# Kernel optimization log

Hardware: AMD Instinct MI355X
Metric: run time of the kernel (lower is better)

The kernel has to match this reference:

```python
import jax, jax.numpy as jnp
import numpy as np

B, S, D = 4, 2048, 384
H, KVH, HD = 6, 2, 64
GROUPS = H // KVH  # 3
ROPE_THETA = 100000.0


def _rope_tables(seq_len, head_dim, theta):
    inv = 1.0 / (theta ** (np.arange(0, head_dim, 2, dtype=np.float32) / head_dim))
    t = np.arange(seq_len, dtype=np.float32)
    freqs = np.outer(t, inv)  # [S, HD//2]
    return jnp.asarray(np.cos(freqs)), jnp.asarray(np.sin(freqs))


def setup_inputs() -> dict:
    key = jax.random.key(0)
    ks = jax.random.split(key, 5)
    hidden_states = jax.random.normal(ks[0], (B, S, D), dtype=jnp.float32)
    Wq = jax.random.normal(ks[1], (D, H * HD), dtype=jnp.float32) * 0.02
    Wk = jax.random.normal(ks[2], (D, KVH * HD), dtype=jnp.float32) * 0.02
    Wv = jax.random.normal(ks[3], (D, KVH * HD), dtype=jnp.float32) * 0.02
    Wo = jax.random.normal(ks[4], (H * HD, D), dtype=jnp.float32) * 0.02
    freqs_cos, freqs_sin = _rope_tables(S, HD, ROPE_THETA)
    return {"hidden_states": hidden_states, "Wq": Wq, "Wk": Wk, "Wv": Wv,
            "Wo": Wo, "freqs_cos": freqs_cos, "freqs_sin": freqs_sin}


def _apply_rope(x, cos, sin):
    # x: [B, S, h, HD]; treat pairs (even, odd) as complex, multiply by e^{i theta}
    xr = x.reshape(*x.shape[:-1], HD // 2, 2)
    x0, x1 = xr[..., 0], xr[..., 1]
    c = cos[None, :, None, :]  # [1, S, 1, HD//2]
    s = sin[None, :, None, :]
    o0 = x0 * c - x1 * s
    o1 = x0 * s + x1 * c
    return jnp.stack([o0, o1], axis=-1).reshape(x.shape)


def reference(hidden_states, Wq, Wk, Wv, Wo, freqs_cos, freqs_sin):
    Bc, Sc, _ = hidden_states.shape
    q = (hidden_states @ Wq).reshape(Bc, Sc, H, HD)
    k = (hidden_states @ Wk).reshape(Bc, Sc, KVH, HD)
    v = (hidden_states @ Wv).reshape(Bc, Sc, KVH, HD)
    q = _apply_rope(q, freqs_cos, freqs_sin)
    k = _apply_rope(k, freqs_cos, freqs_sin)
    # repeat_interleave over the head dim (GQA group broadcast)
    k = jnp.repeat(k, GROUPS, axis=2)  # [B, S, H, HD]
    v = jnp.repeat(v, GROUPS, axis=2)
    scale = 1.0 / jnp.sqrt(jnp.float32(HD))
    scores = jnp.einsum('bqhd,bkhd->bhqk', q, k) * scale  # [B, H, S, S]
    attn = jax.nn.softmax(scores, axis=-1)
    out = jnp.einsum('bhqk,bkhd->bqhd', attn, v)  # [B, S, H, HD]
    out = out.reshape(Bc, Sc, H * HD)
    return out @ Wo
```

## Files before the change

### kernel.cpp

```cpp
#include <hip/hip_runtime.h>
#include <stdint.h>

#define BATCH   4
#define SEQ     2048
#define DMODEL  384
#define NHEAD   6
#define NKVH    2
#define HD      64
#define MTOK    (BATCH*SEQ)
#define NQKV    640
#define QSCALE  (0.125f * 1.4426950408889634f)

typedef __bf16 bf16x8 __attribute__((ext_vector_type(8)));
typedef float  f32x16 __attribute__((ext_vector_type(16)));

__device__ inline unsigned short f2bf(float f) {
  union { float f; unsigned int u; } v; v.f = f;
  return (unsigned short)((v.u + 0x7fffu + ((v.u >> 16) & 1u)) >> 16);
}
__device__ inline float bf2f(unsigned short b) {
  union { unsigned int u; float f; } v; v.u = ((unsigned int)b) << 16;
  return v.f;
}
__device__ inline unsigned int cvtpk(float lo, float hi) {
  unsigned int r;
  asm("v_cvt_pk_bf16_f32 %0, %1, %2" : "=v"(r) : "v"(lo), "v"(hi));
  return r;
}
__device__ inline float exp2_fast(float x) {
  float r;
  asm("v_exp_f32 %0, %1" : "=v"(r) : "v"(x));
  return r;
}

#define GLOAD16(gsrc, ldst) __builtin_amdgcn_global_load_lds( \
    (const __attribute__((address_space(1))) void*)(gsrc), \
    (__attribute__((address_space(3))) void*)(ldst), 16, 0, 0)

__global__ void prep_kernel(const float* __restrict__ X,
                            const float* __restrict__ Wq, const float* __restrict__ Wk,
                            const float* __restrict__ Wv, const float* __restrict__ Wo,
                            unsigned short* __restrict__ Xb,
                            unsigned short* __restrict__ WT,
                            unsigned short* __restrict__ WoT) {
  int idx = blockIdx.x * 256 + threadIdx.x;
  if (idx < (MTOK*DMODEL)/4) {
    float4 v = ((const float4*)X)[idx];
    union { unsigned short s[4]; uint2 u; } o;
    o.s[0] = f2bf(v.x); o.s[1] = f2bf(v.y); o.s[2] = f2bf(v.z); o.s[3] = f2bf(v.w);
    ((uint2*)Xb)[idx] = o.u;
  } else if (idx < (MTOK*DMODEL)/4 + NQKV*DMODEL) {
    int j = idx - (MTOK*DMODEL)/4;
    int n = j / DMODEL, k = j % DMODEL;
    float val = (n < 384) ? Wq[k*384 + n]
              : (n < 512) ? Wk[k*128 + (n-384)]
                          : Wv[k*128 + (n-512)];
    WT[j] = f2bf(val);
  } else if (idx < (MTOK*DMODEL)/4 + NQKV*DMODEL + DMODEL*DMODEL) {
    int j = idx - (MTOK*DMODEL)/4 - NQKV*DMODEL;
    int n = j / DMODEL, k = j % DMODEL;
    WoT[j] = f2bf(Wo[k*384 + n]);
  }
}

template<int NCOLS, bool OUT_BF16, bool ROPE>
__global__ __launch_bounds__(256, 2)
void gemm_kernel(const unsigned short* __restrict__ A,
                 const unsigned short* __restrict__ BT,
                 void* __restrict__ Cout,
                 const float* __restrict__ fcos,
                 const float* __restrict__ fsin) {
  __shared__ unsigned short ldsA[128*64];
  __shared__ unsigned short ldsB[64*64];
  const int tid = threadIdx.x;
  const int wid = tid >> 6, lane = tid & 63;
  const int g = lane >> 5, l31 = lane & 31;
  const int wm = wid >> 1, wn = wid & 1;
  const int mbase = blockIdx.x * 128, nbase = blockIdx.y * 64;

  f32x16 c[2];
  #pragma unroll
  for (int i = 0; i < 2; ++i)
    #pragma unroll
    for (int r = 0; r < 16; ++r) c[i][r] = 0.f;

  for (int kt = 0; kt < DMODEL; kt += 64) {
    #pragma unroll
    for (int i = 0; i < 4; ++i) {
      int L = ((wid*4 + i) << 10) + lane*16;
      int row = L >> 7;
      int slot = (lane & 7) ^ (row & 7);
      GLOAD16(A + (mbase + row)*DMODEL + kt + slot*8, ((char*)ldsA) + L);
    }
    #pragma unroll
    for (int i = 0; i < 2; ++i) {
      int L = ((wid*2 + i) << 10) + lane*16;
      int row = L >> 7;
      int slot = (lane & 7) ^ (row & 7);
      GLOAD16(BT + (nbase + row)*DMODEL + kt + slot*8, ((char*)ldsB) + L);
    }
    __syncthreads();

    bf16x8 bf[4];
    {
      int row = wn*32 + l31;
      #pragma unroll
      for (int s = 0; s < 4; ++s) {
        int slot = ((s<<1) | g) ^ (row & 7);
        bf[s] = *(const bf16x8*)(((const char*)ldsB) + row*128 + slot*16);
      }
    }
    #pragma unroll
    for (int mt = 0; mt < 2; ++mt) {
      int row = wm*64 + mt*32 + l31;
      #pragma unroll
      for (int s = 0; s < 4; ++s) {
        int slot = ((s<<1) | g) ^ (row & 7);
        bf16x8 af = *(const bf16x8*)(((const char*)ldsA) + row*128 + slot*16);
        c[mt] = __builtin_amdgcn_mfma_f32_32x32x16_bf16(af, bf[s], c[mt], 0, 0, 0);
      }
    }
    __syncthreads();
  }

  const int n = nbase + wn*32 + l31;
  const bool isqk = ROPE && (nbase < 512);
  const float rscale = (nbase < 384) ? QSCALE : 1.0f;
  const int ri = (n & 63) >> 1;
  const bool odd = (n & 1) != 0;

  #pragma unroll
  for (int mt = 0; mt < 2; ++mt)
    #pragma unroll
    for (int rr = 0; rr < 16; ++rr) {
      int m = mbase + wm*64 + mt*32 + (rr&3) + ((rr>>2)<<3) + (g<<2);
      float val = c[mt][rr];
      if (isqk) {
        float xp = __shfl_xor(val, 1);
        int s = m & (SEQ-1);
        float cs = fcos[s*32 + ri], sn = fsin[s*32 + ri];
        val = odd ? (xp*sn + val*cs) : (val*cs - xp*sn);
        val *= rscale;
      }
      if (OUT_BF16) ((unsigned short*)Cout)[m*NCOLS + n] = f2bf(val);
      else          ((float*)Cout)[m*NCOLS + n] = val;
    }
}

__global__ void vfrag_kernel(const unsigned short* __restrict__ qkv,
                             unsigned short* __restrict__ Vf) {
  __shared__ unsigned short tile[64][72];
  int t = threadIdx.x;
  int s0 = blockIdx.x * 64;
  int kvh = blockIdx.y;
  int b = blockIdx.z;
  #pragma unroll
  for (int p = 0; p < 2; ++p) {
    int row = (t >> 3) + p*32;
    int c8 = t & 7;
    uint4 v = *(const uint4*)(qkv + (size_t)(b*SEQ + s0 + row)*NQKV + 512 + kvh*64 + c8*8);
    *(uint4*)(&tile[row][c8*8]) = v;
  }
  __syncthreads();
  unsigned short* base = Vf + (size_t)(b*2 + kvh)*131072;
  #pragma unroll
  for (int p = 0; p < 2; ++p) {
    int c = t + p*256;
    int tloc = c >> 8;
    int r = c & 255;
    int dt = r >> 7, sl = (r >> 6) & 1, lane = r & 63;
    int gg = lane >> 5, ll = lane & 31;
    union { unsigned short s[8]; uint4 v; } o;
    #pragma unroll
    for (int j = 0; j < 8; ++j)
      o.s[j] = tile[tloc*32 + sl*16 + gg*8 + j][dt*32 + ll];
    *(uint4*)(base + (size_t)(s0/32 + tloc)*2048 + (dt*2 + sl)*512 + lane*8) = o.v;
  }
}

__device__ __forceinline__ void stage_k(const unsigned short* Kbase, int kv0,
                                        char* kbuf, int lane) {
  #pragma unroll
  for (int i = 0; i < 4; ++i) {
    int L = (i << 10) + lane*16;
    int row = L >> 7;
    int slot = (lane & 7) ^ (row & 7);
    GLOAD16(Kbase + (size_t)(kv0 + row)*NQKV + slot*8, kbuf + L);
  }
}

#define ATTN_BODY(T, VC0, VC1, VC2, VC3, VN0, VN1, VN2, VN3, PREF) do {            \
  if (PREF) {                                                                      \
    stage_k(Kbase, kvbase + ((T)+1)*32, kbuf + (((T)+1)&1)*4096, lane);            \
    const unsigned short* vp = Vfb + (size_t)(part*32 + (T)+1)*2048;               \
    VN0 = *(const bf16x8*)(vp + lane*8);                                           \
    VN1 = *(const bf16x8*)(vp + 512 + lane*8);                                     \
    VN2 = *(const bf16x8*)(vp + 1024 + lane*8);                                    \
    VN3 = *(const bf16x8*)(vp + 1536 + lane*8);                                    \
    asm volatile("s_waitcnt vmcnt(8)" ::: "memory");                               \
  } else {                                                                         \
    asm volatile("s_waitcnt vmcnt(0)" ::: "memory");                               \
  }                                                                                \
  const char* kb = kbuf + ((T)&1)*4096;                                            \
  f32x16 c1;                                                                       \
  _Pragma("unroll")                                                                \
  for (int r = 0; r < 16; ++r) c1[r] = 0.f;                                        \
  _Pragma("unroll")                                                                \
  for (int s = 0; s < 4; ++s) {                                                    \
    int slot = ((s<<1) | g) ^ (l31 & 7);                                           \
    bf16x8 kf = *(const bf16x8*)(kb + l31*128 + slot*16);                          \
    c1 = __builtin_amdgcn_mfma_f32_32x32x16_bf16(kf, qf[s], c1, 0, 0, 0);          \
  }                                                                                \
  float x0 = fmaxf(c1[0],c1[1]), x1 = fmaxf(c1[2],c1[3]);                          \
  float x2 = fmaxf(c1[4],c1[5]), x3 = fmaxf(c1[6],c1[7]);                          \
  float x4 = fmaxf(c1[8],c1[9]), x5 = fmaxf(c1[10],c1[11]);                        \
  float x6 = fmaxf(c1[12],c1[13]), x7 = fmaxf(c1[14],c1[15]);                      \
  float y0 = fmaxf(x0,x1), y1 = fmaxf(x2,x3), y2 = fmaxf(x4,x5), y3 = fmaxf(x6,x7);\
  float pmax = fmaxf(fmaxf(y0,y1), fmaxf(y2,y3));                                  \
  pmax = fmaxf(pmax, __shfl_xor(pmax, 32));                                        \
  if (!__all(pmax <= mrun + 10.f)) {                                               \
    float mnew = fmaxf(mrun, pmax);                                                \
    float alpha = exp2_fast(mrun - mnew);                                          \
    _Pragma("unroll")                                                              \
    for (int r = 0; r < 16; ++r) { acc0[r] *= alpha; acc1[r] *= alpha; }           \
    lrun *= alpha;                                                                 \
    mrun = mnew;                                                                   \
  }                                                                                \
  float p[16];                                                                     \
  _Pragma("unroll")                                                                \
  for (int r = 0; r < 16; ++r) p[r] = exp2_fast(c1[r] - mrun);                     \
  {                                                                                \
    float s0_ = (p[0]+p[1])+(p[2]+p[3]), s1_ = (p[4]+p[5])+(p[6]+p[7]);            \
    float s2_ = (p[8]+p[9])+(p[10]+p[11]), s3_ = (p[12]+p[13])+(p[14]+p[15]);      \
    lrun += (s0_+s1_)+(s2_+s3_);                                                   \
  }                                                                                \
  _Pragma("unroll")                                                                \
  for (int sl = 0; sl < 2; ++sl) {                                                 \
    int rb = sl*8;                                                                 \
    unsigned int w0  = cvtpk(p[rb+0], p[rb+1]);                                    \
    unsigned int w1  = cvtpk(p[rb+2], p[rb+3]);                                    \
    unsigned int wh0 = cvtpk(p[rb+4], p[rb+5]);                                    \
    unsigned int wh1 = cvtpk(p[rb+6], p[rb+7]);                                    \
    unsigned int t0 = g ? w0 : wh0;                                                \
    unsigned int t1 = g ? w1 : wh1;                                                \
    unsigned int r0 = __shfl_xor(t0, 32);                                          \
    unsigned int r1 = __shfl_xor(t1, 32);                                          \
    union { bf16x8 v; unsigned int u[4]; } pf;                                     \
    pf.u[0] = g ? r0  : w0;                                                        \
    pf.u[1] = g ? r1  : w1;                                                        \
    pf.u[2] = g ? wh0 : r0;                                                        \
    pf.u[3] = g ? wh1 : r1;                                                        \
    if (sl == 0) {                                                                 \
      acc0 = __builtin_amdgcn_mfma_f32_32x32x16_bf16(VC0, pf.v, acc0, 0, 0, 0);    \
      acc1 = __builtin_amdgcn_mfma_f32_32x32x16_bf16(VC2, pf.v, acc1, 0, 0, 0);    \
    } else {                                                                       \
      acc0 = __builtin_amdgcn_mfma_f32_32x32x16_bf16(VC1, pf.v, acc0, 0, 0, 0);    \
      acc1 = __builtin_amdgcn_mfma_f32_32x32x16_bf16(VC3, pf.v, acc1, 0, 0, 0);    \
    }                                                                              \
  }                                                                                \
} while (0)

__global__ __launch_bounds__(64, 3)
void attn_kernel(const unsigned short* __restrict__ qkv,
                 const unsigned short* __restrict__ Vf,
                 unsigned short* __restrict__ PO0,
                 unsigned short* __restrict__ PO1,
                 float2* __restrict__ ML) {
  __shared__ __align__(16) char kbuf[8192];
  const int lane = threadIdx.x;
  const int g = lane >> 5, l31 = lane & 31;

  int bid = blockIdx.x;
  const int part = blockIdx.y;
  int e = (bid & 7)*192 + (bid >> 3);
  int qt = e & 63;
  int hb = e >> 6;
  int h = hb % 6, b = hb / 6;
  const int kvh = h / 3;
  const int token = b*SEQ + qt*32 + l31;
  const int kvbase = part * (SEQ/2);

  bf16x8 qf[4];
  #pragma unroll
  for (int s = 0; s < 4; ++s)
    qf[s] = *(const bf16x8*)(qkv + (size_t)token*NQKV + h*64 + s*16 + g*8);

  f32x16 acc0, acc1;
  #pragma unroll
  for (int r = 0; r < 16; ++r) { acc0[r] = 0.f; acc1[r] = 0.f; }
  float mrun = -1e30f, lrun = 0.f;

  const unsigned short* Kbase = qkv + (size_t)(b*SEQ)*NQKV + 384 + kvh*64;
  const unsigned short* Vfb = Vf + (size_t)(b*2 + kvh)*131072;

  bf16x8 vA0, vA1, vA2, vA3, vB0, vB1, vB2, vB3;

  stage_k(Kbase, kvbase, kbuf, lane);
  {
    const unsigned short* vp = Vfb + (size_t)(part*32)*2048;
    vA0 = *(const bf16x8*)(vp + lane*8);
    vA1 = *(const bf16x8*)(vp + 512 + lane*8);
    vA2 = *(const bf16x8*)(vp + 1024 + lane*8);
    vA3 = *(const bf16x8*)(vp + 1536 + lane*8);
  }

  for (int tt = 0; tt < 30; tt += 2) {
    ATTN_BODY(tt,   vA0, vA1, vA2, vA3, vB0, vB1, vB2, vB3, true);
    ATTN_BODY(tt+1, vB0, vB1, vB2, vB3, vA0, vA1, vA2, vA3, true);
  }
  ATTN_BODY(30, vA0, vA1, vA2, vA3, vB0, vB1, vB2, vB3, true);
  ATTN_BODY(31, vB0, vB1, vB2, vB3, vA0, vA1, vA2, vA3, false);

  lrun += __shfl_xor(lrun, 32);
  unsigned short* PO = part ? PO1 : PO0;
  #pragma unroll
  for (int dt = 0; dt < 2; ++dt)
    #pragma unroll
    for (int q8 = 0; q8 < 4; ++q8) {
      union { unsigned short s[4]; uint2 u; } ov;
      #pragma unroll
      for (int j = 0; j < 4; ++j) {
        int r = q8*4 + j;
        ov.s[j] = f2bf(dt ? acc1[r] : acc0[r]);
      }
      int d = dt*32 + q8*8 + g*4;
      *(uint2*)(PO + (size_t)token*DMODEL + h*64 + d) = ov.u;
    }
  if (g == 0)
    ML[(size_t)part*49152 + token*6 + h] = make_float2(mrun, lrun);
}

__global__ void combine_kernel(const unsigned short* __restrict__ PO0,
                               const unsigned short* __restrict__ PO1,
                               const float2* __restrict__ ML,
                               unsigned short* __restrict__ attnO) {
  int idx = blockIdx.x*256 + threadIdx.x;
  int token = idx / 48;
  int c8 = idx - token*48;
  int h = c8 >> 3;
  float2 ml0 = ML[token*6 + h];
  float2 ml1 = ML[49152 + token*6 + h];
  float M = fmaxf(ml0.x, ml1.x);
  float a0 = exp2_fast(ml0.x - M), a1 = exp2_fast(ml1.x - M);
  float inv = 1.0f / (ml0.y*a0 + ml1.y*a1);
  float s0 = a0*inv, s1 = a1*inv;
  union { unsigned short s[8]; uint4 v; } p0, p1, o;
  p0.v = *(const uint4*)(PO0 + (size_t)idx*8);
  p1.v = *(const uint4*)(PO1 + (size_t)idx*8);
  #pragma unroll
  for (int j = 0; j < 8; ++j)
    o.s[j] = f2bf(bf2f(p0.s[j])*s0 + bf2f(p1.s[j])*s1);
  *(uint4*)(attnO + (size_t)idx*8) = o.v;
}

extern "C" void kernel_launch(void* const* d_in, const int* in_sizes, int n_in,
                              void* d_out, int out_size, void* d_ws, size_t ws_size,
                              hipStream_t stream) {
  const float* X    = (const float*)d_in[0];
  const float* Wq   = (const float*)d_in[1];
  const float* Wk   = (const float*)d_in[2];
  const float* Wv   = (const float*)d_in[3];
  const float* Wo   = (const float*)d_in[4];
  const float* fcos = (const float*)d_in[5];
  const float* fsin = (const float*)d_in[6];
  char* ws = (char*)d_ws;

  unsigned short* Xb    = (unsigned short*)(ws);
  unsigned short* PO0   = (unsigned short*)(ws);
  unsigned short* QKV   = (unsigned short*)(ws + 6291456);
  unsigned short* Vf    = (unsigned short*)(ws + 16777216);
  unsigned short* attnO = (unsigned short*)(ws + 18874368);
  unsigned short* WT    = (unsigned short*)(ws + 25165824);
  unsigned short* WoT   = (unsigned short*)(ws + 25657344);
  unsigned short* PO1   = (unsigned short*)(ws + 25952256);
  float2*         ML    = (float2*)       (ws + 32243712);

  prep_kernel<<<4608, 256, 0, stream>>>(X, Wq, Wk, Wv, Wo, Xb, WT, WoT);
  gemm_kernel<NQKV, true, true><<<dim3(64, 10), 256, 0, stream>>>(Xb, WT, QKV, fcos, fsin);
  vfrag_kernel<<<dim3(32, 2, 4), 256, 0, stream>>>(QKV, Vf);
  attn_kernel<<<dim3(1536, 2), 64, 0, stream>>>(QKV, Vf, PO0, PO1, ML);
  combine_kernel<<<1536, 256, 0, stream>>>(PO0, PO1, ML, attnO);
  gemm_kernel<DMODEL, false, false><<<dim3(64, 6), 256, 0, stream>>>(attnO, WoT, (void*)d_out, nullptr, nullptr);
}
```

Before: 155.0 us.

## Fuse split-KV combine into attention via 4-wave blocks reducing in LDS

The attention kernel now uses 256-thread blocks in which each of four waves handles a quarter of the KV sequence for 64 queries, processed as two 32-query subtiles that share each staged K tile and V fragment. The partial softmax states are merged in shared memory and normalized within the block, which removes the separate combine kernel and the global round-trip of the partial outputs and max/sum values. The cost is more registers per wave (two accumulator sets), extra syncthreads and LDS traffic at the end of the kernel, and fewer blocks in the grid.

```diff
diff --git a/kernel.cpp b/kernel.cpp
--- a/kernel.cpp
+++ b/kernel.cpp
@@ -36,6 +36,8 @@
 #define GLOAD16(gsrc, ldst) __builtin_amdgcn_global_load_lds( \
     (const __attribute__((address_space(1))) void*)(gsrc), \
     (__attribute__((address_space(3))) void*)(ldst), 16, 0, 0)
+
+#define WAITVN(n) asm volatile("s_waitcnt vmcnt(" #n ")" ::: "memory")
 
 __global__ void prep_kernel(const float* __restrict__ X,
                             const float* __restrict__ Wq, const float* __restrict__ Wk,
@@ -189,19 +191,7 @@
   }
 }
 
-#define ATTN_BODY(T, VC0, VC1, VC2, VC3, VN0, VN1, VN2, VN3, PREF) do {            \
-  if (PREF) {                                                                      \
-    stage_k(Kbase, kvbase + ((T)+1)*32, kbuf + (((T)+1)&1)*4096, lane);            \
-    const unsigned short* vp = Vfb + (size_t)(part*32 + (T)+1)*2048;               \
-    VN0 = *(const bf16x8*)(vp + lane*8);                                           \
-    VN1 = *(const bf16x8*)(vp + 512 + lane*8);                                     \
-    VN2 = *(const bf16x8*)(vp + 1024 + lane*8);                                    \
-    VN3 = *(const bf16x8*)(vp + 1536 + lane*8);                                    \
-    asm volatile("s_waitcnt vmcnt(8)" ::: "memory");                               \
-  } else {                                                                         \
-    asm volatile("s_waitcnt vmcnt(0)" ::: "memory");                               \
-  }                                                                                \
-  const char* kb = kbuf + ((T)&1)*4096;                                            \
+#define PROC_SUB(QF, MR, LR, AC0, AC1) do {                                        \
   f32x16 c1;                                                                       \
   _Pragma("unroll")                                                                \
   for (int r = 0; r < 16; ++r) c1[r] = 0.f;                                        \
@@ -209,7 +199,7 @@
   for (int s = 0; s < 4; ++s) {                                                    \
     int slot = ((s<<1) | g) ^ (l31 & 7);                                           \
     bf16x8 kf = *(const bf16x8*)(kb + l31*128 + slot*16);                          \
-    c1 = __builtin_amdgcn_mfma_f32_32x32x16_bf16(kf, qf[s], c1, 0, 0, 0);          \
+    c1 = __builtin_amdgcn_mfma_f32_32x32x16_bf16(kf, QF[s], c1, 0, 0, 0);          \
   }                                                                                \
   float x0 = fmaxf(c1[0],c1[1]), x1 = fmaxf(c1[2],c1[3]);                          \
   float x2 = fmaxf(c1[4],c1[5]), x3 = fmaxf(c1[6],c1[7]);                          \
@@ -218,21 +208,21 @@
   float y0 = fmaxf(x0,x1), y1 = fmaxf(x2,x3), y2 = fmaxf(x4,x5), y3 = fmaxf(x6,x7);\
   float pmax = fmaxf(fmaxf(y0,y1), fmaxf(y2,y3));                                  \
   pmax = fmaxf(pmax, __shfl_xor(pmax, 32));                                        \
-  if (!__all(pmax <= mrun + 10.f)) {                                               \
-    float mnew = fmaxf(mrun, pmax);                                                \
-    float alpha = exp2_fast(mrun - mnew);                                          \
+  if (!__all(pmax <= MR + 10.f)) {                                                 \
+    float mnew = fmaxf(MR, pmax);                                                  \
+    float alpha = exp2_fast(MR - mnew);                                            \
     _Pragma("unroll")                                                              \
-    for (int r = 0; r < 16; ++r) { acc0[r] *= alpha; acc1[r] *= alpha; }           \
-    lrun *= alpha;                                                                 \
-    mrun = mnew;                                                                   \
+    for (int r = 0; r < 16; ++r) { AC0[r] *= alpha; AC1[r] *= alpha; }             \
+    LR *= alpha;                                                                   \
+    MR = mnew;                                                                     \
   }                                                                                \
   float p[16];                                                                     \
   _Pragma("unroll")                                                                \
-  for (int r = 0; r < 16; ++r) p[r] = exp2_fast(c1[r] - mrun);                     \
+  for (int r = 0; r < 16; ++r) p[r] = exp2_fast(c1[r] - MR);                       \
   {                                                                                \
     float s0_ = (p[0]+p[1])+(p[2]+p[3]), s1_ = (p[4]+p[5])+(p[6]+p[7]);            \
     float s2_ = (p[8]+p[9])+(p[10]+p[11]), s3_ = (p[12]+p[13])+(p[14]+p[15]);      \
-    lrun += (s0_+s1_)+(s2_+s3_);                                                   \
+    LR += (s0_+s1_)+(s2_+s3_);                                                     \
   }                                                                                \
   _Pragma("unroll")                                                                \
   for (int sl = 0; sl < 2; ++sl) {                                                 \
@@ -251,106 +241,139 @@
     pf.u[2] = g ? wh0 : r0;                                                        \
     pf.u[3] = g ? wh1 : r1;                                                        \
     if (sl == 0) {                                                                 \
-      acc0 = __builtin_amdgcn_mfma_f32_32x32x16_bf16(VC0, pf.v, acc0, 0, 0, 0);    \
-      acc1 = __builtin_amdgcn_mfma_f32_32x32x16_bf16(VC2, pf.v, acc1, 0, 0, 0);    \
+      AC0 = __builtin_amdgcn_mfma_f32_32x32x16_bf16(vC0, pf.v, AC0, 0, 0, 0);      \
+      AC1 = __builtin_amdgcn_mfma_f32_32x32x16_bf16(vC2, pf.v, AC1, 0, 0, 0);      \
     } else {                                                                       \
-      acc0 = __builtin_amdgcn_mfma_f32_32x32x16_bf16(VC1, pf.v, acc0, 0, 0, 0);    \
-      acc1 = __builtin_amdgcn_mfma_f32_32x32x16_bf16(VC3, pf.v, acc1, 0, 0, 0);    \
+      AC0 = __builtin_amdgcn_mfma_f32_32x32x16_bf16(vC1, pf.v, AC0, 0, 0, 0);      \
+      AC1 = __builtin_amdgcn_mfma_f32_32x32x16_bf16(vC3, pf.v, AC1, 0, 0, 0);      \
     }                                                                              \
   }                                                                                \
 } while (0)
 
-__global__ __launch_bounds__(64, 3)
+__global__ __launch_bounds__(256, 3)
 void attn_kernel(const unsigned short* __restrict__ qkv,
                  const unsigned short* __restrict__ Vf,
-                 unsigned short* __restrict__ PO0,
-                 unsigned short* __restrict__ PO1,
-                 float2* __restrict__ ML) {
-  __shared__ __align__(16) char kbuf[8192];
-  const int lane = threadIdx.x;
+                 unsigned short* __restrict__ attnO) {
+  __shared__ __align__(16) char smem[32768];
+  const int tid = threadIdx.x;
+  const int wid = tid >> 6, lane = tid & 63;
   const int g = lane >> 5, l31 = lane & 31;
 
   int bid = blockIdx.x;
-  const int part = blockIdx.y;
-  int e = (bid & 7)*192 + (bid >> 3);
-  int qt = e & 63;
-  int hb = e >> 6;
+  int e = (bid & 7)*96 + (bid >> 3);
+  int qt = e & 31;
+  int hb = e >> 5;
   int h = hb % 6, b = hb / 6;
   const int kvh = h / 3;
-  const int token = b*SEQ + qt*32 + l31;
-  const int kvbase = part * (SEQ/2);
-
-  bf16x8 qf[4];
-  #pragma unroll
-  for (int s = 0; s < 4; ++s)
-    qf[s] = *(const bf16x8*)(qkv + (size_t)token*NQKV + h*64 + s*16 + g*8);
-
-  f32x16 acc0, acc1;
-  #pragma unroll
-  for (int r = 0; r < 16; ++r) { acc0[r] = 0.f; acc1[r] = 0.f; }
-  float mrun = -1e30f, lrun = 0.f;
+  const int tokA = b*SEQ + qt*64 + l31;
+  const int tokB = tokA + 32;
+  const int kvbase = wid * 512;
+
+  char* kb0 = smem + wid*8192;
+
+  bf16x8 qfA[4], qfB[4];
+  #pragma unroll
+  for (int s = 0; s < 4; ++s) {
+    qfA[s] = *(const bf16x8*)(qkv + (size_t)tokA*NQKV + h*64 + s*16 + g*8);
+    qfB[s] = *(const bf16x8*)(qkv + (size_t)tokB*NQKV + h*64 + s*16 + g*8);
+  }
+
+  f32x16 aA0, aA1, aB0, aB1;
+  #pragma unroll
+  for (int r = 0; r < 16; ++r) { aA0[r] = 0.f; aA1[r] = 0.f; aB0[r] = 0.f; aB1[r] = 0.f; }
+  float mA = -1e30f, lA = 0.f, mB = -1e30f, lB = 0.f;
 
   const unsigned short* Kbase = qkv + (size_t)(b*SEQ)*NQKV + 384 + kvh*64;
   const unsigned short* Vfb = Vf + (size_t)(b*2 + kvh)*131072;
 
-  bf16x8 vA0, vA1, vA2, vA3, vB0, vB1, vB2, vB3;
-
-  stage_k(Kbase, kvbase, kbuf, lane);
-  {
-    const unsigned short* vp = Vfb + (size_t)(part*32)*2048;
-    vA0 = *(const bf16x8*)(vp + lane*8);
-    vA1 = *(const bf16x8*)(vp + 512 + lane*8);
-    vA2 = *(const bf16x8*)(vp + 1024 + lane*8);
-    vA3 = *(const bf16x8*)(vp + 1536 + lane*8);
-  }
-
-  for (int tt = 0; tt < 30; tt += 2) {
-    ATTN_BODY(tt,   vA0, vA1, vA2, vA3, vB0, vB1, vB2, vB3, true);
-    ATTN_BODY(tt+1, vB0, vB1, vB2, vB3, vA0, vA1, vA2, vA3, true);
-  }
-  ATTN_BODY(30, vA0, vA1, vA2, vA3, vB0, vB1, vB2, vB3, true);
-  ATTN_BODY(31, vB0, vB1, vB2, vB3, vA0, vA1, vA2, vA3, false);
-
-  lrun += __shfl_xor(lrun, 32);
-  unsigned short* PO = part ? PO1 : PO0;
-  #pragma unroll
-  for (int dt = 0; dt < 2; ++dt)
-    #pragma unroll
-    for (int q8 = 0; q8 < 4; ++q8) {
-      union { unsigned short s[4]; uint2 u; } ov;
+  stage_k(Kbase, kvbase, kb0, lane);
+
+  bf16x8 vC0, vC1, vC2, vC3;
+  for (int t = 0; t < 16; ++t) {
+    const bool pref = (t < 15);
+    {
+      const unsigned short* vp = Vfb + (size_t)(wid*16 + t)*2048 + lane*8;
+      vC0 = *(const bf16x8*)(vp);
+      vC1 = *(const bf16x8*)(vp + 512);
+      vC2 = *(const bf16x8*)(vp + 1024);
+      vC3 = *(const bf16x8*)(vp + 1536);
+    }
+    __builtin_amdgcn_sched_barrier(0);
+    if (pref) {
+      stage_k(Kbase, kvbase + (t+1)*32, kb0 + ((t+1)&1)*4096, lane);
+      WAITVN(8);
+    } else {
+      WAITVN(4);
+    }
+    const char* kb = kb0 + (t&1)*4096;
+    PROC_SUB(qfA, mA, lA, aA0, aA1);
+    PROC_SUB(qfB, mB, lB, aB0, aB1);
+  }
+
+  lA += __shfl_xor(lA, 32);
+  lB += __shfl_xor(lB, 32);
+  __syncthreads();
+  float* cmb  = (float*)(smem + 24576);
+  float* slab = (float*)smem;
+  if (g == 0) {
+    cmb[((wid*2+0)*2+0)*32 + l31] = mA;
+    cmb[((wid*2+0)*2+1)*32 + l31] = lA;
+    cmb[((wid*2+1)*2+0)*32 + l31] = mB;
+    cmb[((wid*2+1)*2+1)*32 + l31] = lB;
+  }
+  __syncthreads();
+  #pragma unroll
+  for (int sub = 0; sub < 2; ++sub) {
+    float m0 = cmb[((0*2+sub)*2+0)*32 + l31];
+    float m1 = cmb[((1*2+sub)*2+0)*32 + l31];
+    float m2 = cmb[((2*2+sub)*2+0)*32 + l31];
+    float m3 = cmb[((3*2+sub)*2+0)*32 + l31];
+    float M = fmaxf(fmaxf(m0, m1), fmaxf(m2, m3));
+    float msub = sub ? mB : mA;
+    float aw = exp2_fast(msub - M);
+    f32x16 u0 = sub ? aB0 : aA0;
+    f32x16 u1 = sub ? aB1 : aA1;
+    if (wid != 0) {
+      float* s = slab + (wid-1)*2048;
       #pragma unroll
-      for (int j = 0; j < 4; ++j) {
-        int r = q8*4 + j;
-        ov.s[j] = f2bf(dt ? acc1[r] : acc0[r]);
-      }
-      int d = dt*32 + q8*8 + g*4;
-      *(uint2*)(PO + (size_t)token*DMODEL + h*64 + d) = ov.u;
-    }
-  if (g == 0)
-    ML[(size_t)part*49152 + token*6 + h] = make_float2(mrun, lrun);
-}
-
-__global__ void combine_kernel(const unsigned short* __restrict__ PO0,
-                               const unsigned short* __restrict__ PO1,
-                               const float2* __restrict__ ML,
-                               unsigned short* __restrict__ attnO) {
-  int idx = blockIdx.x*256 + threadIdx.x;
-  int token = idx / 48;
-  int c8 = idx - token*48;
-  int h = c8 >> 3;
-  float2 ml0 = ML[token*6 + h];
-  float2 ml1 = ML[49152 + token*6 + h];
-  float M = fmaxf(ml0.x, ml1.x);
-  float a0 = exp2_fast(ml0.x - M), a1 = exp2_fast(ml1.x - M);
-  float inv = 1.0f / (ml0.y*a0 + ml1.y*a1);
-  float s0 = a0*inv, s1 = a1*inv;
-  union { unsigned short s[8]; uint4 v; } p0, p1, o;
-  p0.v = *(const uint4*)(PO0 + (size_t)idx*8);
-  p1.v = *(const uint4*)(PO1 + (size_t)idx*8);
-  #pragma unroll
-  for (int j = 0; j < 8; ++j)
-    o.s[j] = f2bf(bf2f(p0.s[j])*s0 + bf2f(p1.s[j])*s1);
-  *(uint4*)(attnO + (size_t)idx*8) = o.v;
+      for (int dt = 0; dt < 2; ++dt)
+        #pragma unroll
+        for (int r = 0; r < 16; ++r) {
+          int d = dt*32 + (r&3) + ((r>>2)<<3) + (g<<2);
+          s[d*32 + l31] = (dt ? u1[r] : u0[r]) * aw;
+        }
+    }
+    __syncthreads();
+    if (wid == 0) {
+      float l0 = cmb[((0*2+sub)*2+1)*32 + l31];
+      float l1 = cmb[((1*2+sub)*2+1)*32 + l31];
+      float l2 = cmb[((2*2+sub)*2+1)*32 + l31];
+      float l3 = cmb[((3*2+sub)*2+1)*32 + l31];
+      float lsum = l0*exp2_fast(m0-M) + l1*exp2_fast(m1-M)
+                 + l2*exp2_fast(m2-M) + l3*exp2_fast(m3-M);
+      float invl = 1.0f / lsum;
+      int token = sub ? tokB : tokA;
+      #pragma unroll
+      for (int dt = 0; dt < 2; ++dt)
+        #pragma unroll
+        for (int q8 = 0; q8 < 4; ++q8) {
+          union { unsigned short s[4]; uint2 u; } ov;
+          #pragma unroll
+          for (int j = 0; j < 4; ++j) {
+            int r = q8*4 + j;
+            int d = dt*32 + (r&3) + ((r>>2)<<3) + (g<<2);
+            float tot = (dt ? u1[r] : u0[r]) * aw
+                      + slab[0*2048 + d*32 + l31]
+                      + slab[1*2048 + d*32 + l31]
+                      + slab[2*2048 + d*32 + l31];
+            ov.s[j] = f2bf(tot * invl);
+          }
+          int d0 = dt*32 + q8*8 + g*4;
+          *(uint2*)(attnO + (size_t)token*DMODEL + h*64 + d0) = ov.u;
+        }
+    }
+    __syncthreads();
+  }
 }
 
 extern "C" void kernel_launch(void* const* d_in, const int* in_sizes, int n_in,
@@ -366,19 +389,15 @@
   char* ws = (char*)d_ws;
 
   unsigned short* Xb    = (unsigned short*)(ws);
-  unsigned short* PO0   = (unsigned short*)(ws);
+  unsigned short* attnO = (unsigned short*)(ws);
   unsigned short* QKV   = (unsigned short*)(ws + 6291456);
   unsigned short* Vf    = (unsigned short*)(ws + 16777216);
-  unsigned short* attnO = (unsigned short*)(ws + 18874368);
-  unsigned short* WT    = (unsigned short*)(ws + 25165824);
-  unsigned short* WoT   = (unsigned short*)(ws + 25657344);
-  unsigned short* PO1   = (unsigned short*)(ws + 25952256);
-  float2*         ML    = (float2*)       (ws + 32243712);
+  unsigned short* WT    = (unsigned short*)(ws + 18874368);
+  unsigned short* WoT   = (unsigned short*)(ws + 19365888);
 
   prep_kernel<<<4608, 256, 0, stream>>>(X, Wq, Wk, Wv, Wo, Xb, WT, WoT);
   gemm_kernel<NQKV, true, true><<<dim3(64, 10), 256, 0, stream>>>(Xb, WT, QKV, fcos, fsin);
   vfrag_kernel<<<dim3(32, 2, 4), 256, 0, stream>>>(QKV, Vf);
-  attn_kernel<<<dim3(1536, 2), 64, 0, stream>>>(QKV, Vf, PO0, PO1, ML);
-  combine_kernel<<<1536, 256, 0, stream>>>(PO0, PO1, ML, attnO);
+  attn_kernel<<<768, 256, 0, stream>>>(QKV, Vf, attnO);
   gemm_kernel<DMODEL, false, false><<<dim3(64, 6), 256, 0, stream>>>(attnO, WoT, (void*)d_out, nullptr, nullptr);
 }
```

After: 166.6 us. +7.5%, slower.
